# Kernel optimization log

Measured on AMD Instinct MI355X. Metric: run time of the kernel, lower is better.

## Reference

```python
import jax, jax.numpy as jnp
import numpy as np

NBINS = 64
EPS = 1e-10
SIGMA = 1.0 / (NBINS - 1)


def setup_inputs() -> dict:
    key = jax.random.key(0)
    k1, k2 = jax.random.split(key)
    pred = jax.random.normal(k1, (8, 1, 512, 512), dtype=jnp.float32)
    target = jax.random.normal(k2, (8, 1, 512, 512), dtype=jnp.float32)
    return {"pred": pred, "target": target}


def _normalize(x):
    # per-sample min-max normalization to [0,1]
    B = x.shape[0]
    xf = x.reshape(B, -1)
    x_min = xf.min(axis=1, keepdims=True)
    x_max = xf.max(axis=1, keepdims=True)
    return (xf - x_min) / (x_max - x_min + EPS)  # (B, Npix)


def reference(pred, target):
    B = pred.shape[0]
    Npix = pred.shape[-2] * pred.shape[-1]
    centers = jnp.linspace(0.0, 1.0, NBINS, dtype=jnp.float32)  # (nbins,)

    pred_flat = _normalize(pred)      # (B, Npix)
    tgt_flat = _normalize(target)     # (B, Npix)

    inv2s2 = 1.0 / (2.0 * SIGMA * SIGMA)
    # Gaussian soft-binning weights: (B, Npix, nbins)
    w_pred = jnp.exp(-(pred_flat[:, :, None] - centers) ** 2 * inv2s2)
    w_tgt = jnp.exp(-(tgt_flat[:, :, None] - centers) ** 2 * inv2s2)

    # joint histogram via batched contraction over pixels: (B, nbins, nbins)
    p_xy = jnp.einsum('bni,bnj->bij', w_pred, w_tgt) / float(Npix)
    p_x = p_xy.sum(axis=2)  # (B, nbins)
    p_y = p_xy.sum(axis=1)  # (B, nbins)

    px_py = p_x[:, :, None] * p_y[:, None, :]
    ratio = (p_xy + EPS) / (px_py + EPS)
    mi = (p_xy * jnp.log(ratio)).sum(axis=(1, 2))  # (B,)
    return -mi.mean()
```

## Files before the change

### kernel.cpp

```cpp
#include <hip/hip_runtime.h>
#include <stdint.h>

#define NPIX  (512 * 512)
#define NB    8
#define NCH   32
#define CHPX  (NPIX / NCH)
#define FB    128
#define MPW   161
#define HDR_FLOATS 1024

typedef __attribute__((ext_vector_type(4))) unsigned uint4v;
typedef __attribute__((ext_vector_type(4))) float    float4v;

__device__ constexpr float WK[33] = {
  1.2664166e-14f, 6.1019365e-13f, 2.2897490e-11f, 6.6915858e-10f,
  1.5229979e-08f, 2.6995785e-07f, 3.7266532e-06f, 4.0065297e-05f,
  3.3546263e-04f, 2.1874911e-03f, 1.1108997e-02f, 4.3936934e-02f,
  1.3533528e-01f, 3.2465247e-01f, 6.0653066e-01f, 8.8249690e-01f,
  1.0f,
  8.8249690e-01f, 6.0653066e-01f, 3.2465247e-01f, 1.3533528e-01f,
  4.3936934e-02f, 1.1108997e-02f, 2.1874911e-03f, 3.3546263e-04f,
  4.0065297e-05f, 3.7266532e-06f, 2.6995785e-07f, 1.5229979e-08f,
  6.6915858e-10f, 2.2897490e-11f, 6.1019365e-13f, 1.2664166e-14f
};

__global__ __launch_bounds__(1024) void minmax_kernel(const float* __restrict__ pred,
                                                      const float* __restrict__ tgt,
                                                      float2* __restrict__ mm) {
  __shared__ float smin[16], smax[16];
  const int tid = threadIdx.x, lane = tid & 63, wave = tid >> 6;
  const int pair = blockIdx.x >> 4, sub = blockIdx.x & 15;
  const float* src = pair < 8 ? pred + (size_t)pair * NPIX
                              : tgt  + (size_t)(pair - 8) * NPIX;
  const float4v* s4 = (const float4v*)src + sub * 4096;
  float vmin = 3.0e38f, vmax = -3.0e38f;
  #pragma unroll
  for (int k = 0; k < 4; ++k) {
    float4v v = s4[k * 1024 + tid];
    vmin = fminf(vmin, fminf(fminf(v[0], v[1]), fminf(v[2], v[3])));
    vmax = fmaxf(vmax, fmaxf(fmaxf(v[0], v[1]), fmaxf(v[2], v[3])));
  }
  #pragma unroll
  for (int off = 32; off; off >>= 1) {
    vmin = fminf(vmin, __shfl_xor(vmin, off));
    vmax = fmaxf(vmax, __shfl_xor(vmax, off));
  }
  if (lane == 0) { smin[wave] = vmin; smax[wave] = vmax; }
  __syncthreads();
  if (tid == 0) {
    float m = smin[0], M = smax[0];
    #pragma unroll
    for (int w = 1; w < 16; ++w) { m = fminf(m, smin[w]); M = fmaxf(M, smax[w]); }
    mm[blockIdx.x] = (float2){m, M};
  }
}

__global__ __launch_bounds__(512) void fine_hist_kernel(const float* __restrict__ pred,
                                                        const float* __restrict__ tgt,
                                                        const float2* __restrict__ mm,
                                                        unsigned* __restrict__ part) {
  __shared__ unsigned H[FB * FB / 2];
  const int tid = threadIdx.x;
  const int b = blockIdx.x >> 5, c = blockIdx.x & 31;

  float pmin = 3.0e38f, pmax = -3.0e38f, tmin = 3.0e38f, tmax = -3.0e38f;
  #pragma unroll
  for (int s2 = 0; s2 < 16; ++s2) {
    float2 a = mm[b * 16 + s2], d = mm[(8 + b) * 16 + s2];
    pmin = fminf(pmin, a.x); pmax = fmaxf(pmax, a.y);
    tmin = fminf(tmin, d.x); tmax = fmaxf(tmax, d.y);
  }
  const float sp = 126.0f / (pmax - pmin + 1e-10f), op = -pmin * sp + 0.5f;
  const float st = 126.0f / (tmax - tmin + 1e-10f), ot = -tmin * st + 0.5f;

  #pragma unroll
  for (int j = 0; j < 4; ++j)
    ((uint4v*)H)[j * 512 + tid] = (uint4v){0u, 0u, 0u, 0u};
  __syncthreads();

  const float4v* p4 = (const float4v*)(pred + (size_t)b * NPIX + (size_t)c * CHPX);
  const float4v* t4 = (const float4v*)(tgt  + (size_t)b * NPIX + (size_t)c * CHPX);
  #pragma unroll
  for (int it = 0; it < 4; ++it) {
    float4v vp = p4[it * 512 + tid];
    float4v vt = t4[it * 512 + tid];
    #pragma unroll
    for (int j = 0; j < 4; ++j) {
      int fp = (int)(vp[j] * sp + op);
      int ft = (int)(vt[j] * st + ot);
      atomicAdd(&H[(fp << 6) | (ft >> 1)], 1u << ((ft & 1) << 4));
    }
  }
  __syncthreads();

  uint4v* dst = (uint4v*)(part + ((size_t)blockIdx.x << 13));
  #pragma unroll
  for (int j = 0; j < 4; ++j)
    dst[j * 512 + tid] = ((uint4v*)H)[j * 512 + tid];
}

__global__ __launch_bounds__(256) void reduce_fine_kernel(const unsigned* __restrict__ part,
                                                          float2* __restrict__ fineF) {
  const int tid = threadIdx.x;
  const int b = blockIdx.x >> 5, sl = blockIdx.x & 31;
  const int w = sl * 256 + tid;
  const unsigned* src = part + ((size_t)b << 18) + w;
  unsigned lo = 0, hi = 0;
  #pragma unroll 8
  for (int c = 0; c < 32; ++c) {
    unsigned v = src[(size_t)c << 13];
    lo += v & 0xFFFFu; hi += v >> 16;
  }
  float2 o; o.x = (float)lo; o.y = (float)hi;
  fineF[(size_t)b * 8192 + w] = o;
}

__global__ __launch_bounds__(256) void conv1_kernel(const float* __restrict__ fineG,
                                                    float* __restrict__ midP) {
  __shared__ float T[47 * 128];
  const int tid = threadIdx.x;
  const int b = blockIdx.x >> 3, ig = blockIdx.x & 7;
  const int fp0 = 16 * ig - 16;

  #pragma unroll
  for (int ii = 0; ii < 24; ++ii) {
    int idx = ii * 256 + tid;
    if (idx < 47 * 128) {
      int tr = idx >> 7, ft = idx & 127, fp = fp0 + tr;
      T[idx] = ((unsigned)fp < 128u) ? fineG[((size_t)b << 14) + (fp << 7) + ft] : 0.0f;
    }
  }
  __syncthreads();

  const int ft = tid & 127, ih = tid >> 7;
  float v[39];
  #pragma unroll
  for (int t = 0; t < 39; ++t) v[t] = T[(ih * 8 + t) * 128 + ft];
  float acc[4] = {0.0f, 0.0f, 0.0f, 0.0f};
  #pragma unroll
  for (int d = 0; d < 4; ++d)
    #pragma unroll
    for (int k = 0; k < 33; ++k) acc[d] += WK[k] * v[2 * d + k];

  float* mb = midP + (size_t)b * (64 * MPW);
  #pragma unroll
  for (int d = 0; d < 4; ++d)
    mb[(8 * ig + ih * 4 + d) * MPW + ft + 16] = acc[d];
  for (int idx = tid; idx < 8 * 33; idx += 256) {
    int rr = idx / 33, cc = idx % 33;
    int col = cc < 16 ? cc : cc + 128;
    mb[(8 * ig + rr) * MPW + col] = 0.0f;
  }
}

__global__ __launch_bounds__(1024) void conv2mi_kernel(const float* __restrict__ midP,
                                                       float* __restrict__ mi_out) {
  __shared__ float S[14608];
  const int tid = threadIdx.x, lane = tid & 63, wave = tid >> 6;
  const int b = blockIdx.x;

  const float* mb = midP + (size_t)b * (64 * MPW);
  #pragma unroll
  for (int ii = 0; ii < 11; ++ii) {
    int idx = ii * 1024 + tid;
    if (idx < 64 * MPW) S[idx] = mb[idx];
  }
  __syncthreads();

  const int i = tid & 63, js = (tid >> 6) << 2;
  {
    float v[39];
    #pragma unroll
    for (int t = 0; t < 39; ++t) v[t] = S[i * MPW + 2 * js + t];
    float acc[4] = {0.0f, 0.0f, 0.0f, 0.0f};
    #pragma unroll
    for (int d = 0; d < 4; ++d)
      #pragma unroll
      for (int k = 0; k < 33; ++k) acc[d] += WK[k] * v[2 * d + k];
    const float invN = 1.0f / (float)NPIX;
    #pragma unroll
    for (int d = 0; d < 4; ++d) S[10304 + i * 65 + js + d] = acc[d] * invN;
  }
  __syncthreads();

  {
    const int l16 = lane & 15, sub16 = lane >> 4;
    int row = 4 * wave + sub16;
    float s = 0.0f;
    #pragma unroll
    for (int k = 0; k < 4; ++k) s += S[10304 + row * 65 + l16 * 4 + k];
    #pragma unroll
    for (int off = 8; off; off >>= 1) s += __shfl_xor(s, off);
    if (l16 == 0) S[14464 + row] = s;
    float t2 = 0.0f;
    #pragma unroll
    for (int k = 0; k < 4; ++k) t2 += S[10304 + (l16 * 4 + k) * 65 + row];
    #pragma unroll
    for (int off = 8; off; off >>= 1) t2 += __shfl_xor(t2, off);
    if (l16 == 0) S[14528 + row] = t2;
  }
  __syncthreads();

  float a = 0.0f;
  #pragma unroll
  for (int r = 0; r < 4; ++r) {
    int e = r * 1024 + tid;
    int ii = e >> 6, jj = e & 63;
    float pv = S[10304 + ii * 65 + jj];
    float d = S[14464 + ii] * S[14528 + jj] + 1e-10f;
    a += pv * __logf((pv + 1e-10f) / d);
  }
  #pragma unroll
  for (int off = 32; off; off >>= 1) a += __shfl_xor(a, off);
  if (lane == 0) S[14592 + wave] = a;
  __syncthreads();
  if (tid == 0) {
    float s = 0.0f;
    #pragma unroll
    for (int w = 0; w < 16; ++w) s += S[14592 + w];
    mi_out[b] = s;
  }
}

__global__ void final_kernel(const float* __restrict__ mi, float* __restrict__ out) {
  if (threadIdx.x == 0) {
    float s = 0.0f;
    #pragma unroll
    for (int b = 0; b < NB; ++b) s += mi[b];
    out[0] = -(s * (1.0f / NB));
  }
}

extern "C" void kernel_launch(void* const* d_in, const int* in_sizes, int n_in,
                              void* d_out, int out_size, void* d_ws, size_t ws_size,
                              hipStream_t stream) {
  const float* pred = (const float*)d_in[0];
  const float* tgt  = (const float*)d_in[1];
  float*    out  = (float*)d_out;
  float*    wsf  = (float*)d_ws;
  float2*   mm   = (float2*)d_ws;
  float*    mi   = wsf + 512;
  unsigned* part = (unsigned*)(wsf + HDR_FLOATS);
  float*    fineG = wsf + HDR_FLOATS + (size_t)NB * NCH * 8192;
  float*    midP  = fineG + (size_t)NB * 16384;

  minmax_kernel     <<<256,      1024, 0, stream>>>(pred, tgt, mm);
  fine_hist_kernel  <<<NB * NCH,  512, 0, stream>>>(pred, tgt, mm, part);
  reduce_fine_kernel<<<256,       256, 0, stream>>>(part, (float2*)fineG);
  conv1_kernel      <<<NB * 8,    256, 0, stream>>>(fineG, midP);
  conv2mi_kernel    <<<NB,       1024, 0, stream>>>(midP, mi);
  final_kernel      <<<1,          64, 0, stream>>>(mi, out);
}
```

Before: 31.82 us.

## Fuse conv1, conv2+MI and final reduction into one tail kernel; swizzle histogram LDS

Merges the first Gaussian convolution pass, the second pass with the MI computation, and the final batch mean into a single tail kernel. The last block to finish, detected with an atomic counter that the minmax kernel resets, writes the output. This removes two kernel launches and the midP round-trip through global memory. In exchange only 8 blocks do the conv1 work, with 47 global loads per thread. The fine histogram's shared-memory word index is also XOR-swizzled by fp to spread atomic bank conflicts, and the write-out unswizzles it.

```diff
diff --git a/kernel.cpp b/kernel.cpp
--- a/kernel.cpp
+++ b/kernel.cpp
@@ -26,9 +26,11 @@
 
 __global__ __launch_bounds__(1024) void minmax_kernel(const float* __restrict__ pred,
                                                       const float* __restrict__ tgt,
-                                                      float2* __restrict__ mm) {
+                                                      float2* __restrict__ mm,
+                                                      unsigned* __restrict__ cnt) {
   __shared__ float smin[16], smax[16];
   const int tid = threadIdx.x, lane = tid & 63, wave = tid >> 6;
+  if (blockIdx.x == 0 && tid == 0) cnt[0] = 0u;
   const int pair = blockIdx.x >> 4, sub = blockIdx.x & 15;
   const float* src = pair < 8 ? pred + (size_t)pair * NPIX
                               : tgt  + (size_t)(pair - 8) * NPIX;
@@ -88,15 +90,18 @@
     for (int j = 0; j < 4; ++j) {
       int fp = (int)(vp[j] * sp + op);
       int ft = (int)(vt[j] * st + ot);
-      atomicAdd(&H[(fp << 6) | (ft >> 1)], 1u << ((ft & 1) << 4));
+      int w  = (fp << 6) | (ft >> 1);
+      atomicAdd(&H[w ^ ((fp & 7) << 2)], 1u << ((ft & 1) << 4));
     }
   }
   __syncthreads();
 
   uint4v* dst = (uint4v*)(part + ((size_t)blockIdx.x << 13));
   #pragma unroll
-  for (int j = 0; j < 4; ++j)
-    dst[j * 512 + tid] = ((uint4v*)H)[j * 512 + tid];
+  for (int j = 0; j < 4; ++j) {
+    int g = j * 512 + tid;
+    dst[g] = ((uint4v*)H)[g ^ ((g >> 4) & 7)];
+  }
 }
 
 __global__ __launch_bounds__(256) void reduce_fine_kernel(const unsigned* __restrict__ part,
@@ -115,55 +120,43 @@
   fineF[(size_t)b * 8192 + w] = o;
 }
 
-__global__ __launch_bounds__(256) void conv1_kernel(const float* __restrict__ fineG,
-                                                    float* __restrict__ midP) {
-  __shared__ float T[47 * 128];
-  const int tid = threadIdx.x;
-  const int b = blockIdx.x >> 3, ig = blockIdx.x & 7;
-  const int fp0 = 16 * ig - 16;
-
-  #pragma unroll
-  for (int ii = 0; ii < 24; ++ii) {
-    int idx = ii * 256 + tid;
-    if (idx < 47 * 128) {
-      int tr = idx >> 7, ft = idx & 127, fp = fp0 + tr;
-      T[idx] = ((unsigned)fp < 128u) ? fineG[((size_t)b << 14) + (fp << 7) + ft] : 0.0f;
-    }
-  }
-  __syncthreads();
-
-  const int ft = tid & 127, ih = tid >> 7;
-  float v[39];
-  #pragma unroll
-  for (int t = 0; t < 39; ++t) v[t] = T[(ih * 8 + t) * 128 + ft];
-  float acc[4] = {0.0f, 0.0f, 0.0f, 0.0f};
-  #pragma unroll
-  for (int d = 0; d < 4; ++d)
-    #pragma unroll
-    for (int k = 0; k < 33; ++k) acc[d] += WK[k] * v[2 * d + k];
-
-  float* mb = midP + (size_t)b * (64 * MPW);
-  #pragma unroll
-  for (int d = 0; d < 4; ++d)
-    mb[(8 * ig + ih * 4 + d) * MPW + ft + 16] = acc[d];
-  for (int idx = tid; idx < 8 * 33; idx += 256) {
-    int rr = idx / 33, cc = idx % 33;
-    int col = cc < 16 ? cc : cc + 128;
-    mb[(8 * ig + rr) * MPW + col] = 0.0f;
-  }
-}
-
-__global__ __launch_bounds__(1024) void conv2mi_kernel(const float* __restrict__ midP,
-                                                       float* __restrict__ mi_out) {
+__global__ __launch_bounds__(1024) void tail_kernel(const float* __restrict__ fineG,
+                                                    float* __restrict__ mi,
+                                                    unsigned* __restrict__ cnt,
+                                                    float* __restrict__ out) {
   __shared__ float S[14608];
   const int tid = threadIdx.x, lane = tid & 63, wave = tid >> 6;
   const int b = blockIdx.x;
 
-  const float* mb = midP + (size_t)b * (64 * MPW);
-  #pragma unroll
-  for (int ii = 0; ii < 11; ++ii) {
-    int idx = ii * 1024 + tid;
-    if (idx < 64 * MPW) S[idx] = mb[idx];
+  {
+    const int ft = tid & 127, r = tid >> 7;
+    const float* fb = fineG + ((size_t)b << 14) + ft;
+    float v[47];
+    #pragma unroll
+    for (int t = 0; t < 47; ++t) {
+      int fp = 16 * r - 16 + t;
+      v[t] = ((unsigned)fp < 128u) ? fb[fp << 7] : 0.0f;
+    }
+    float acc[8];
+    #pragma unroll
+    for (int d = 0; d < 8; ++d) {
+      float a = 0.0f;
+      #pragma unroll
+      for (int k = 0; k < 33; ++k) a += WK[k] * v[2 * d + k];
+      acc[d] = a;
+    }
+    #pragma unroll
+    for (int d = 0; d < 8; ++d)
+      S[(8 * r + d) * MPW + ft + 16] = acc[d];
+    #pragma unroll
+    for (int ii = 0; ii < 3; ++ii) {
+      int idx = ii * 1024 + tid;
+      if (idx < 64 * 33) {
+        int rr = idx / 33, cc = idx % 33;
+        int col = cc < 16 ? cc : cc + 128;
+        S[rr * MPW + col] = 0.0f;
+      }
+    }
   }
   __syncthreads();
 
@@ -214,20 +207,22 @@
   for (int off = 32; off; off >>= 1) a += __shfl_xor(a, off);
   if (lane == 0) S[14592 + wave] = a;
   __syncthreads();
+
   if (tid == 0) {
     float s = 0.0f;
     #pragma unroll
     for (int w = 0; w < 16; ++w) s += S[14592 + w];
-    mi_out[b] = s;
-  }
-}
-
-__global__ void final_kernel(const float* __restrict__ mi, float* __restrict__ out) {
-  if (threadIdx.x == 0) {
-    float s = 0.0f;
-    #pragma unroll
-    for (int b = 0; b < NB; ++b) s += mi[b];
-    out[0] = -(s * (1.0f / NB));
+    atomicExch(&mi[b], s);
+    __threadfence();
+    unsigned prev = atomicAdd(cnt, 1u);
+    if (prev == NB - 1) {
+      __threadfence();
+      float tot = 0.0f;
+      #pragma unroll
+      for (int k = 0; k < NB; ++k) tot += atomicAdd(&mi[k], 0.0f);
+      out[0] = -(tot * (1.0f / NB));
+      atomicExch(cnt, 0u);
+    }
   }
 }
 
@@ -240,14 +235,12 @@
   float*    wsf  = (float*)d_ws;
   float2*   mm   = (float2*)d_ws;
   float*    mi   = wsf + 512;
+  unsigned* cnt  = (unsigned*)(wsf + 520);
   unsigned* part = (unsigned*)(wsf + HDR_FLOATS);
   float*    fineG = wsf + HDR_FLOATS + (size_t)NB * NCH * 8192;
-  float*    midP  = fineG + (size_t)NB * 16384;
-
-  minmax_kernel     <<<256,      1024, 0, stream>>>(pred, tgt, mm);
+
+  minmax_kernel     <<<256,      1024, 0, stream>>>(pred, tgt, mm, cnt);
   fine_hist_kernel  <<<NB * NCH,  512, 0, stream>>>(pred, tgt, mm, part);
   reduce_fine_kernel<<<256,       256, 0, stream>>>(part, (float2*)fineG);
-  conv1_kernel      <<<NB * 8,    256, 0, stream>>>(fineG, midP);
-  conv2mi_kernel    <<<NB,       1024, 0, stream>>>(midP, mi);
-  final_kernel      <<<1,          64, 0, stream>>>(mi, out);
-}
+  tail_kernel       <<<NB,       1024, 0, stream>>>(fineG, mi, cnt, out);
+}
```

New measurement: 29.32 us. 7.8% less time.
